# Kernel tuning notes

Hardware: AMD Instinct MI355X
Metric: run time of the kernel (lower is better)

The kernel has to match this reference:

```python
import math
import jax, jax.numpy as jnp
import numpy as np

DIM = 128
NUM_PROJ = 256
ENC = jnp.asarray(2 ** np.arange(8), dtype=jnp.uint8)  # [1,2,4,...,128]
DEQUANT_SCALE = math.sqrt(math.pi / 2) / NUM_PROJ


def quantize_packed(x, S):
    # x: (..., dim) float32 -> packed uint8 (..., ceil(num_proj/8))
    projected = jnp.einsum('...d,pd->...p', x, S)
    signs = projected > 0  # bool (..., num_proj)
    pad_len = (-NUM_PROJ) % 8
    if pad_len > 0:
        pad = [(0, 0)] * (signs.ndim - 1) + [(0, pad_len)]
        signs = jnp.pad(signs, pad, constant_values=False)
    signs = signs.reshape(*signs.shape[:-1], -1, 8)  # (..., nbytes, 8)
    packed = jnp.sum(signs.astype(jnp.uint8) * ENC, axis=-1, dtype=jnp.uint8)
    return packed


def unpack_signs(packed):
    # packed: uint8 (..., nbytes) -> {-1,+1} float32 (..., num_proj)
    bits = jnp.bitwise_and(packed[..., None], ENC) > 0  # (..., nbytes, 8)
    bits = bits.reshape(*packed.shape[:-1], -1)[..., :NUM_PROJ]
    return bits.astype(jnp.float32) * 2.0 - 1.0


def setup_inputs() -> dict:
    key = jax.random.key(0)
    k1, k2, k3 = jax.random.split(key, 3)
    query = jax.random.normal(k1, (2, 32, 4096, DIM), dtype=jnp.float32)
    key_t = jax.random.normal(k2, (2, 32, 4096, DIM), dtype=jnp.float32)
    S = jax.random.normal(k3, (NUM_PROJ, DIM), dtype=jnp.float32)
    return {"query": query, "key": key_t, "S": S}


def reference(query, key, S):
    # quantize keys to bit-packed sign sketch, then estimate <query, key>
    packed = quantize_packed(key, S)                       # uint8 (..., 32)
    signs = unpack_signs(packed)                           # (..., 256)
    q_proj = jnp.einsum('...d,pd->...p', query, S)         # (..., 256)
    est = DEQUANT_SCALE * jnp.sum(q_proj * signs, axis=-1) # (B,H,S)
    return est
```

## Files before the change

### kernel.cpp

```cpp
#include <hip/hip_runtime.h>
#include <stdint.h>

#define DIM 128
#define NPROJ 256
#define TPB 64
#define TAU 0.016f
#define QCAP 512
#define DEQ 0.004895758348888673f

typedef _Float16 f16x8 __attribute__((ext_vector_type(8)));
typedef float f32x4 __attribute__((ext_vector_type(4)));

__global__ __launch_bounds__(256) void qjl_prep(const float* __restrict__ Sg,
                                                _Float16* __restrict__ ws) {
    int t = blockIdx.x * 256 + threadIdx.x;
    int lane = t & 63, fid = t >> 6;
    int f = fid & 1, ks = (fid >> 1) & 3, c = fid >> 3;
    int p = c * 32 + f * 16 + (lane & 15);
    int d0 = ks * 32 + (lane >> 4) * 8;
    const float4* s4 = (const float4*)(Sg + p * DIM + d0);
    float4 a = s4[0], b = s4[1];
    f16x8 h = {(_Float16)a.x, (_Float16)a.y, (_Float16)a.z, (_Float16)a.w,
               (_Float16)b.x, (_Float16)b.y, (_Float16)b.z, (_Float16)b.w};
    *(f16x8*)(ws + (size_t)fid * 512 + lane * 8) = h;
}

#define LOADT(buf, C, T)                                                             \
    { _Pragma("unroll")                                                              \
      for (int ks = 0; ks < 4; ++ks)                                                 \
          buf[ks] = *(const f16x8*)(bs + ((C) * 8 + ks * 2 + (T)) * 512 + lane * 8); }

#define LOADA(dst, src)                                                              \
    { const float* rp = (src) + (tok0 + wv * 16 + m) * DIM;                          \
      _Pragma("unroll")                                                              \
      for (int ks = 0; ks < 4; ++ks) {                                               \
          int d0 = ks * 32 + quad * 8;                                               \
          float4 x = *(const float4*)(rp + d0);                                      \
          float4 y = *(const float4*)(rp + d0 + 4);                                  \
          dst[ks] = (f16x8){(_Float16)x.x, (_Float16)x.y, (_Float16)x.z, (_Float16)x.w, \
                            (_Float16)y.x, (_Float16)y.y, (_Float16)y.z, (_Float16)y.w}; } }

#define F_STEP(C, T, buf)                                                            \
    { f32x4 k0 = {0,0,0,0}, q0 = {0,0,0,0};                                          \
      _Pragma("unroll")                                                              \
      for (int ks = 0; ks < 4; ++ks) {                                               \
          k0 = __builtin_amdgcn_mfma_f32_16x16x32_f16(ak[ks], buf[ks], k0, 0,0,0);   \
          q0 = __builtin_amdgcn_mfma_f32_16x16x32_f16(aq[ks], buf[ks], q0, 0,0,0);   \
      }                                                                              \
      _Pragma("unroll")                                                              \
      for (int r = 0; r < 4; ++r) {                                                  \
          uint32_t s0 = __float_as_uint(k0[r]) & 0x80000000u;                        \
          est[r] += __uint_as_float(__float_as_uint(q0[r]) ^ s0);                    \
          if (__builtin_expect(fabsf(k0[r]) < TAU, 0)) {                             \
              int idx = atomicAdd(&qn, 1);                                           \
              if (idx < QCAP) qmeta[idx] = (uint32_t)(wv * 16 + quad * 4 + r)        \
                  | ((uint32_t)((C) * 32 + (T) * 16 + m) << 8)                       \
                  | ((s0 ? 0u : 1u) << 16);                                          \
          } } }

__global__ __launch_bounds__(256, 2) void qjl_main(
    const float* __restrict__ qg, const float* __restrict__ kg,
    const float* __restrict__ Sg, const _Float16* __restrict__ ws,
    float* __restrict__ out)
{
    __shared__ _Float16 bs[32768];
    __shared__ float    est_s[TPB];
    __shared__ uint32_t qmeta[QCAP];
    __shared__ int      qn;

    const int tid = threadIdx.x, lane = tid & 63, wv = tid >> 6;
    const int m = lane & 15, quad = lane >> 4;
    const long tok0 = (long)blockIdx.x * TPB;
    if (tid == 0) qn = 0;

    {
        const char* gsrc = (const char*)ws + tid * 16;
        char* ldst = (char*)bs + tid * 16;
        #pragma unroll
        for (int r = 0; r < 16; ++r)
            __builtin_amdgcn_global_load_lds(
                (const __attribute__((address_space(1))) void*)(gsrc + r * 4096),
                (__attribute__((address_space(3))) void*)(ldst + r * 4096),
                16, 0, 0);
    }

    f16x8 ak[4], aq[4];
    f16x8 tA[4], tB[4];
    float est[4] = {0.f, 0.f, 0.f, 0.f};

    LOADA(ak, kg);
    LOADA(aq, qg);
    __syncthreads();

    LOADT(tA, 0, 0);
    LOADT(tB, 0, 1);
    F_STEP(0, 0, tA); LOADT(tA, 1, 0);
    F_STEP(0, 1, tB); LOADT(tB, 1, 1);
    F_STEP(1, 0, tA); LOADT(tA, 2, 0);
    F_STEP(1, 1, tB); LOADT(tB, 2, 1);
    F_STEP(2, 0, tA); LOADT(tA, 3, 0);
    F_STEP(2, 1, tB); LOADT(tB, 3, 1);
    F_STEP(3, 0, tA); LOADT(tA, 4, 0);
    F_STEP(3, 1, tB); LOADT(tB, 4, 1);
    F_STEP(4, 0, tA); LOADT(tA, 5, 0);
    F_STEP(4, 1, tB); LOADT(tB, 5, 1);
    F_STEP(5, 0, tA); LOADT(tA, 6, 0);
    F_STEP(5, 1, tB); LOADT(tB, 6, 1);
    F_STEP(6, 0, tA); LOADT(tA, 7, 0);
    F_STEP(6, 1, tB); LOADT(tB, 7, 1);
    F_STEP(7, 0, tA);
    F_STEP(7, 1, tB);

    #pragma unroll
    for (int r = 0; r < 4; ++r) {
        float e = est[r];
        e += __shfl_xor(e, 1);
        e += __shfl_xor(e, 2);
        e += __shfl_xor(e, 4);
        e += __shfl_xor(e, 8);
        if (m == 0) est_s[wv * 16 + quad * 4 + r] = DEQ * e;
    }
    __syncthreads();

    int nc = qn < QCAP ? qn : QCAP;
    for (int i = tid; i < nc; i += 256) {
        uint32_t mm = qmeta[i];
        int tl = mm & 255;
        int p  = (mm >> 8) & 255;
        int sf = (mm >> 16) & 1;
        const float4* kr = (const float4*)(kg + (tok0 + tl) * DIM);
        const float4* qr = (const float4*)(qg + (tok0 + tl) * DIM);
        const float4* sr = (const float4*)(Sg + (long)p * DIM);
        double dk = 0.0, dq = 0.0;
        #pragma unroll 8
        for (int j = 0; j < 32; ++j) {
            float4 kv4 = kr[j], qv4 = qr[j], sv4 = sr[j];
            dk += (double)kv4.x * (double)sv4.x + (double)kv4.y * (double)sv4.y
                + (double)kv4.z * (double)sv4.z + (double)kv4.w * (double)sv4.w;
            dq += (double)qv4.x * (double)sv4.x + (double)qv4.y * (double)sv4.y
                + (double)qv4.z * (double)sv4.z + (double)qv4.w * (double)sv4.w;
        }
        int st = (dk > 0.0) ? 1 : 0;
        if (st != sf) {
            float sg = sf ? 1.f : -1.f;
            atomicAdd(&est_s[tl], -2.f * DEQ * (float)dq * sg);
        }
    }
    __syncthreads();

    if (tid < TPB) out[tok0 + tid] = est_s[tid];
}

extern "C" void kernel_launch(void* const* d_in, const int* in_sizes, int n_in,
                              void* d_out, int out_size, void* d_ws, size_t ws_size,
                              hipStream_t stream) {
    const float* q = (const float*)d_in[0];
    const float* k = (const float*)d_in[1];
    const float* S = (const float*)d_in[2];
    float* out = (float*)d_out;
    _Float16* ws = (_Float16*)d_ws;
    hipLaunchKernelGGL(qjl_prep, dim3(16), dim3(256), 0, stream, S, ws);
    int nblocks = out_size / TPB;
    hipLaunchKernelGGL(qjl_main, dim3(nblocks), dim3(256), 0, stream, q, k, S, ws, out);
}
```

Measured before the change: 313.6 us.

## Make main kernel persistent with per-wave sign-fix queues and cooperative recheck

The main kernel becomes persistent: 512 blocks loop over 64-token tiles, so the S sketch is loaded into LDS once per block instead of once per tile. Near-zero projections are queued per wave along with the fp16 q projection value. Each queued item is then rechecked in double precision by the whole wave using a shuffle reduction, and the correction is applied with a global atomic on the output. This cuts the repeated LDS staging and the block-wide barriers. In exchange the correction uses the fp16 q projection rather than an exact one, the fallback no longer recomputes it, and the output is written twice with atomics on flagged tokens.

```diff
diff --git a/kernel.cpp b/kernel.cpp
--- a/kernel.cpp
+++ b/kernel.cpp
@@ -3,10 +3,10 @@
 
 #define DIM 128
 #define NPROJ 256
-#define TPB 64
 #define TAU 0.016f
-#define QCAP 512
+#define QCAPW 64
 #define DEQ 0.004895758348888673f
+#define NBLK 512
 
 typedef _Float16 f16x8 __attribute__((ext_vector_type(8)));
 typedef float f32x4 __attribute__((ext_vector_type(4)));
@@ -25,10 +25,10 @@
     *(f16x8*)(ws + (size_t)fid * 512 + lane * 8) = h;
 }
 
-#define LOADT(buf, C, T)                                                             \
+#define LOADT(dst, C, T)                                                             \
     { _Pragma("unroll")                                                              \
       for (int ks = 0; ks < 4; ++ks)                                                 \
-          buf[ks] = *(const f16x8*)(bs + ((C) * 8 + ks * 2 + (T)) * 512 + lane * 8); }
+          dst[ks] = *(const f16x8*)(bs + ((C) * 8 + ks * 2 + (T)) * 512 + lane * 8); }
 
 #define LOADA(dst, src)                                                              \
     { const float* rp = (src) + (tok0 + wv * 16 + m) * DIM;                          \
@@ -52,26 +52,27 @@
           uint32_t s0 = __float_as_uint(k0[r]) & 0x80000000u;                        \
           est[r] += __uint_as_float(__float_as_uint(q0[r]) ^ s0);                    \
           if (__builtin_expect(fabsf(k0[r]) < TAU, 0)) {                             \
-              int idx = atomicAdd(&qn, 1);                                           \
-              if (idx < QCAP) qmeta[idx] = (uint32_t)(wv * 16 + quad * 4 + r)        \
-                  | ((uint32_t)((C) * 32 + (T) * 16 + m) << 8)                       \
-                  | ((s0 ? 0u : 1u) << 16);                                          \
+              int idx = atomicAdd(&qn[wv], 1);                                       \
+              if (idx < QCAPW) {                                                     \
+                  qmeta[wv][idx] = (uint32_t)(quad * 4 + r)                          \
+                      | ((uint32_t)((C) * 32 + (T) * 16 + m) << 4)                   \
+                      | ((s0 ? 0u : 1u) << 12);                                      \
+                  qval[wv][idx] = q0[r];                                             \
+              }                                                                      \
           } } }
 
 __global__ __launch_bounds__(256, 2) void qjl_main(
     const float* __restrict__ qg, const float* __restrict__ kg,
     const float* __restrict__ Sg, const _Float16* __restrict__ ws,
-    float* __restrict__ out)
+    float* __restrict__ out, int ntiles)
 {
     __shared__ _Float16 bs[32768];
-    __shared__ float    est_s[TPB];
-    __shared__ uint32_t qmeta[QCAP];
-    __shared__ int      qn;
+    __shared__ uint32_t qmeta[4][QCAPW];
+    __shared__ float    qval[4][QCAPW];
+    __shared__ int      qn[4];
 
     const int tid = threadIdx.x, lane = tid & 63, wv = tid >> 6;
     const int m = lane & 15, quad = lane >> 4;
-    const long tok0 = (long)blockIdx.x * TPB;
-    if (tid == 0) qn = 0;
 
     {
         const char* gsrc = (const char*)ws + tid * 16;
@@ -83,72 +84,73 @@
                 (__attribute__((address_space(3))) void*)(ldst + r * 4096),
                 16, 0, 0);
     }
+    __syncthreads();
 
     f16x8 ak[4], aq[4];
     f16x8 tA[4], tB[4];
-    float est[4] = {0.f, 0.f, 0.f, 0.f};
 
-    LOADA(ak, kg);
-    LOADA(aq, qg);
-    __syncthreads();
+    for (int tile = blockIdx.x; tile < ntiles; tile += NBLK) {
+        const long tok0 = (long)tile * 64;
+        if (lane == 0) qn[wv] = 0;
 
-    LOADT(tA, 0, 0);
-    LOADT(tB, 0, 1);
-    F_STEP(0, 0, tA); LOADT(tA, 1, 0);
-    F_STEP(0, 1, tB); LOADT(tB, 1, 1);
-    F_STEP(1, 0, tA); LOADT(tA, 2, 0);
-    F_STEP(1, 1, tB); LOADT(tB, 2, 1);
-    F_STEP(2, 0, tA); LOADT(tA, 3, 0);
-    F_STEP(2, 1, tB); LOADT(tB, 3, 1);
-    F_STEP(3, 0, tA); LOADT(tA, 4, 0);
-    F_STEP(3, 1, tB); LOADT(tB, 4, 1);
-    F_STEP(4, 0, tA); LOADT(tA, 5, 0);
-    F_STEP(4, 1, tB); LOADT(tB, 5, 1);
-    F_STEP(5, 0, tA); LOADT(tA, 6, 0);
-    F_STEP(5, 1, tB); LOADT(tB, 6, 1);
-    F_STEP(6, 0, tA); LOADT(tA, 7, 0);
-    F_STEP(6, 1, tB); LOADT(tB, 7, 1);
-    F_STEP(7, 0, tA);
-    F_STEP(7, 1, tB);
+        LOADA(ak, kg);
+        LOADA(aq, qg);
+        float est[4] = {0.f, 0.f, 0.f, 0.f};
 
-    #pragma unroll
-    for (int r = 0; r < 4; ++r) {
-        float e = est[r];
-        e += __shfl_xor(e, 1);
-        e += __shfl_xor(e, 2);
-        e += __shfl_xor(e, 4);
-        e += __shfl_xor(e, 8);
-        if (m == 0) est_s[wv * 16 + quad * 4 + r] = DEQ * e;
-    }
-    __syncthreads();
+        LOADT(tA, 0, 0);
+        LOADT(tB, 0, 1);
+        F_STEP(0, 0, tA); LOADT(tA, 1, 0);
+        F_STEP(0, 1, tB); LOADT(tB, 1, 1);
+        F_STEP(1, 0, tA); LOADT(tA, 2, 0);
+        F_STEP(1, 1, tB); LOADT(tB, 2, 1);
+        F_STEP(2, 0, tA); LOADT(tA, 3, 0);
+        F_STEP(2, 1, tB); LOADT(tB, 3, 1);
+        F_STEP(3, 0, tA); LOADT(tA, 4, 0);
+        F_STEP(3, 1, tB); LOADT(tB, 4, 1);
+        F_STEP(4, 0, tA); LOADT(tA, 5, 0);
+        F_STEP(4, 1, tB); LOADT(tB, 5, 1);
+        F_STEP(5, 0, tA); LOADT(tA, 6, 0);
+        F_STEP(5, 1, tB); LOADT(tB, 6, 1);
+        F_STEP(6, 0, tA); LOADT(tA, 7, 0);
+        F_STEP(6, 1, tB); LOADT(tB, 7, 1);
+        F_STEP(7, 0, tA);
+        F_STEP(7, 1, tB);
 
-    int nc = qn < QCAP ? qn : QCAP;
-    for (int i = tid; i < nc; i += 256) {
-        uint32_t mm = qmeta[i];
-        int tl = mm & 255;
-        int p  = (mm >> 8) & 255;
-        int sf = (mm >> 16) & 1;
-        const float4* kr = (const float4*)(kg + (tok0 + tl) * DIM);
-        const float4* qr = (const float4*)(qg + (tok0 + tl) * DIM);
-        const float4* sr = (const float4*)(Sg + (long)p * DIM);
-        double dk = 0.0, dq = 0.0;
-        #pragma unroll 8
-        for (int j = 0; j < 32; ++j) {
-            float4 kv4 = kr[j], qv4 = qr[j], sv4 = sr[j];
-            dk += (double)kv4.x * (double)sv4.x + (double)kv4.y * (double)sv4.y
-                + (double)kv4.z * (double)sv4.z + (double)kv4.w * (double)sv4.w;
-            dq += (double)qv4.x * (double)sv4.x + (double)qv4.y * (double)sv4.y
-                + (double)qv4.z * (double)sv4.z + (double)qv4.w * (double)sv4.w;
+        #pragma unroll
+        for (int r = 0; r < 4; ++r) {
+            float e = est[r];
+            e += __shfl_xor(e, 1);
+            e += __shfl_xor(e, 2);
+            e += __shfl_xor(e, 4);
+            e += __shfl_xor(e, 8);
+            est[r] = DEQ * e;
         }
-        int st = (dk > 0.0) ? 1 : 0;
-        if (st != sf) {
-            float sg = sf ? 1.f : -1.f;
-            atomicAdd(&est_s[tl], -2.f * DEQ * (float)dq * sg);
+        if (m == 0) {
+            float4 o = {est[0], est[1], est[2], est[3]};
+            *(float4*)(out + tok0 + wv * 16 + quad * 4) = o;
+        }
+        asm volatile("s_waitcnt vmcnt(0) lgkmcnt(0)" ::: "memory");
+
+        int nc = qn[wv] < QCAPW ? qn[wv] : QCAPW;
+        for (int i = 0; i < nc; ++i) {
+            uint32_t mm = qmeta[wv][i];
+            int tl = mm & 15;
+            int p  = (mm >> 4) & 255;
+            int sf = (mm >> 12) & 1;
+            const float2* kr = (const float2*)(kg + (tok0 + wv * 16 + tl) * DIM);
+            const float2* sr = (const float2*)(Sg + (long)p * DIM);
+            float2 kv = kr[lane], sv = sr[lane];
+            double d = (double)kv.x * (double)sv.x + (double)kv.y * (double)sv.y;
+            #pragma unroll
+            for (int off = 1; off < 64; off <<= 1)
+                d += __shfl_xor(d, off);
+            int st = (d > 0.0) ? 1 : 0;
+            if (st != sf && lane == 0) {
+                float sg = sf ? 1.f : -1.f;
+                atomicAdd(&out[tok0 + wv * 16 + tl], -2.f * DEQ * qval[wv][i] * sg);
+            }
         }
     }
-    __syncthreads();
-
-    if (tid < TPB) out[tok0 + tid] = est_s[tid];
 }
 
 extern "C" void kernel_launch(void* const* d_in, const int* in_sizes, int n_in,
@@ -160,6 +162,6 @@
     float* out = (float*)d_out;
     _Float16* ws = (_Float16*)d_ws;
     hipLaunchKernelGGL(qjl_prep, dim3(16), dim3(256), 0, stream, S, ws);
-    int nblocks = out_size / TPB;
-    hipLaunchKernelGGL(qjl_main, dim3(nblocks), dim3(256), 0, stream, q, k, S, ws, out);
+    int ntiles = out_size / 64;
+    hipLaunchKernelGGL(qjl_main, dim3(NBLK), dim3(256), 0, stream, q, k, S, ws, out, ntiles);
 }
```

Measured after the change: 297.7 us. -5.0%, faster.
